# Optimization experiments

Measured on AMD Instinct MI355X. Metric: run time of the kernel, lower is better.

Reference implementation:

```python
import jax, jax.numpy as jnp
import numpy as np

EPS = 1e-7

def sphere_log(p, q):
    # Riemannian log on unit sphere; p, q broadcastable, points along last axis.
    dot = jnp.clip(jnp.sum(p * q, axis=-1, keepdims=True), -1.0 + EPS, 1.0 - EPS)
    theta = jnp.arccos(dot)
    v = q - dot * p                      # tangent direction (unnormalized)
    nv = jnp.linalg.norm(v, axis=-1, keepdims=True)
    nv_safe = jnp.where(nv < EPS, 1.0, nv)
    factor = jnp.where(nv < EPS, 1.0, theta / nv_safe)  # theta/||v|| -> 1 as q->p
    return factor * v

def sphere_exp(p, v):
    # Riemannian exp on unit sphere.
    n = jnp.linalg.norm(v, axis=-1, keepdims=True)
    n_safe = jnp.where(n < EPS, 1.0, n)
    s = jnp.where(n < EPS, 1.0, jnp.sin(n_safe) / n_safe)  # sinc(||v||)
    return jnp.cos(n) * p + s * v

def setup_inputs() -> dict:
    key = jax.random.key(0)
    k1, k2 = jax.random.split(key)
    B, L, C_in, C_out, d = 4, 256, 64, 64, 64
    x = jax.random.normal(k1, (B, L, C_in, d), dtype=jnp.float32)
    x = x / jnp.linalg.norm(x, axis=-1, keepdims=True)  # points on S^{d-1}
    # param 'w': truncated_normal(stddev=1) with shape (n_in, n_out)
    w_raw = jax.random.truncated_normal(k2, -2.0, 2.0, (C_in, C_out), dtype=jnp.float32)
    return {"x": x, "w_raw": w_raw}

def reference(x, w_raw):
    B, L, C_in, d = x.shape
    C_out = w_raw.shape[1]
    # softmax-like positive, column-normalized weights
    w = jnp.exp(w_raw - np.log(C_in).astype(np.float32))
    w = w / w.sum(axis=0)[None]          # (C_in, C_out)

    xr = x.reshape(B * L, C_in, d)       # (N, C_in, d)
    # init at first in-channel point, broadcast over out channels: (N, C_out, d)
    a = jnp.broadcast_to(xr[:, 0][:, None, :], (B * L, C_out, d))

    # 3-step fixed-point iteration toward weighted Frechet mean (scan unroll=3)
    for _ in range(3):
        logs = sphere_log(a[:, :, None, :], xr[:, None, :, :])  # (N, C_out, C_in, d)
        grad = jnp.einsum('io,noid->nod', w, logs)              # (N, C_out, d)
        a = sphere_exp(a, grad)

    return a.reshape(B, L, C_out, d)
```

## Files before the change

kernel.cpp:

```cpp
#include <hip/hip_runtime.h>

#define EPSF 1e-7f
#define TS2 72

typedef __bf16 bf16;
typedef __attribute__((ext_vector_type(8))) __bf16 bf16x8;
typedef __attribute__((ext_vector_type(4))) __bf16 bf16x4;
typedef __attribute__((ext_vector_type(4))) float f32x4;

__device__ __forceinline__ float dpp_sum16(float v) {
  int x;
  x = __builtin_amdgcn_update_dpp(0, __builtin_bit_cast(int, v), 0xB1, 0xf, 0xf, true);
  v += __builtin_bit_cast(float, x);
  x = __builtin_amdgcn_update_dpp(0, __builtin_bit_cast(int, v), 0x4E, 0xf, 0xf, true);
  v += __builtin_bit_cast(float, x);
  x = __builtin_amdgcn_update_dpp(0, __builtin_bit_cast(int, v), 0x141, 0xf, 0xf, true);
  v += __builtin_bit_cast(float, x);
  x = __builtin_amdgcn_update_dpp(0, __builtin_bit_cast(int, v), 0x140, 0xf, 0xf, true);
  v += __builtin_bit_cast(float, x);
  return v;
}

__device__ __forceinline__ float fused_factor(float dot) {
  float ax = fabsf(dot);
  float q2 = __builtin_amdgcn_rsqf(1.0f + ax);
  float r2 = __builtin_amdgcn_rsqf(1.0f - ax);
  float pa = fmaf(fmaf(fmaf(-0.0187292994f, ax, 0.0742610070f), ax,
                       -0.2121144013f), ax, 1.5707288f);
  float sel = (dot < 0.0f) ? fmaf(3.14159265358979f, r2, -pa) : pa;
  return sel * q2;
}

__global__ __launch_bounds__(256, 4) void mfd_fc_mfma(
    const float* __restrict__ x, const float* __restrict__ wraw,
    float* __restrict__ out) {
  __shared__ __align__(16) char smem[3 * 64 * TS2 * sizeof(bf16)];
  bf16* Xrow = (bf16*)smem;
  bf16* Xt   = Xrow + 64 * TS2;
  bf16* AC   = Xt + 64 * TS2;

  const int n = blockIdx.x;
  const int tid = threadIdx.x;
  const int wv = tid >> 6;
  const int lane = tid & 63;
  const int ln15 = lane & 15;
  const int quad = lane >> 4;
  const int obase = 16 * wv + 4 * quad;
  const float* xn = x + (size_t)n * 4096;

#pragma unroll
  for (int t = 0; t < 4; ++t) {
    int idx = tid + t * 256;
    int i = idx >> 4;
    int c4 = (idx & 15) << 2;
    float4 v = reinterpret_cast<const float4*>(xn)[idx];
    bf16x4 b;
    b[0] = (bf16)v.x; b[1] = (bf16)v.y; b[2] = (bf16)v.z; b[3] = (bf16)v.w;
    *reinterpret_cast<bf16x4*>(&Xrow[i * TS2 + c4]) = b;
  }

  float wf[4][4];
  {
    float cs[4] = {0.f, 0.f, 0.f, 0.f};
#pragma unroll
    for (int t = 0; t < 4; ++t) {
      float4 wr = *reinterpret_cast<const float4*>(&wraw[(16 * t + ln15) * 64 + obase]);
      wf[t][0] = __expf(wr.x); wf[t][1] = __expf(wr.y);
      wf[t][2] = __expf(wr.z); wf[t][3] = __expf(wr.w);
#pragma unroll
      for (int r = 0; r < 4; ++r) cs[r] += wf[t][r];
    }
#pragma unroll
    for (int r = 0; r < 4; ++r) {
      float inv = __builtin_amdgcn_rcpf(dpp_sum16(cs[r]));
#pragma unroll
      for (int t = 0; t < 4; ++t) wf[t][r] *= inv;
    }
  }

  float a_reg[4][4];
#pragma unroll
  for (int t = 0; t < 4; ++t) {
    float v = xn[16 * t + ln15];
#pragma unroll
    for (int r = 0; r < 4; ++r) a_reg[t][r] = v;
  }

  __syncthreads();

  bf16x8 xrf[4][2];
#pragma unroll
  for (int t = 0; t < 4; ++t)
#pragma unroll
    for (int ks = 0; ks < 2; ++ks)
      xrf[t][ks] = *reinterpret_cast<const bf16x8*>(
          &Xrow[(16 * t + ln15) * TS2 + ks * 32 + quad * 8]);

  bf16x8 x0f[2];
#pragma unroll
  for (int ks = 0; ks < 2; ++ks)
    x0f[ks] = *reinterpret_cast<const bf16x8*>(&Xrow[ks * 32 + quad * 8]);

  {
    int dd = tid & 63, ih = tid >> 6;
    bf16 tmp[16];
#pragma unroll
    for (int j = 0; j < 16; ++j) tmp[j] = Xrow[(16 * ih + j) * TS2 + dd];
    *reinterpret_cast<bf16x8*>(&Xt[dd * TS2 + 16 * ih]) =
        *reinterpret_cast<bf16x8*>(&tmp[0]);
    *reinterpret_cast<bf16x8*>(&Xt[dd * TS2 + 16 * ih + 8]) =
        *reinterpret_cast<bf16x8*>(&tmp[8]);
  }

  const bf16* acbase = &AC[(16 * wv + ln15) * TS2];

  for (int it = 0; it < 3; ++it) {
    float sd[4] = {0.f, 0.f, 0.f, 0.f};
    if (it == 0) {
#pragma unroll
      for (int t = 0; t < 4; ++t) {
        float p = 0.f;
#pragma unroll
        for (int ks = 0; ks < 2; ++ks)
#pragma unroll
          for (int j = 0; j < 8; ++j)
            p = fmaf((float)xrf[t][ks][j], (float)x0f[ks][j], p);
        p += __shfl_xor(p, 16, 64);
        p += __shfl_xor(p, 32, 64);
        float d0 = __builtin_amdgcn_fmed3f(p, -1.0f + EPSF, 1.0f - EPSF);
        float f0 = fused_factor(d0);
#pragma unroll
        for (int r = 0; r < 4; ++r) {
          bf16 cb = (bf16)(wf[t][r] * f0);
          AC[(obase + r) * TS2 + 16 * t + ln15] = cb;
          sd[r] = fmaf((float)cb, d0, sd[r]);
        }
      }
    } else {
      f32x4 acc[4] = {f32x4{0,0,0,0}, f32x4{0,0,0,0}, f32x4{0,0,0,0}, f32x4{0,0,0,0}};
#pragma unroll
      for (int ks = 0; ks < 2; ++ks) {
        bf16x8 af = *reinterpret_cast<const bf16x8*>(&acbase[ks * 32 + quad * 8]);
#pragma unroll
        for (int t = 0; t < 4; ++t)
          acc[t] = __builtin_amdgcn_mfma_f32_16x16x32_bf16(af, xrf[t][ks], acc[t], 0, 0, 0);
      }
#pragma unroll
      for (int t = 0; t < 4; ++t) {
#pragma unroll
        for (int r = 0; r < 4; ++r) {
          float raw = acc[t][r];
          float dot = __builtin_amdgcn_fmed3f(raw, -1.0f + EPSF, 1.0f - EPSF);
          bf16 cb = (bf16)(wf[t][r] * fused_factor(dot));
          AC[(obase + r) * TS2 + 16 * t + ln15] = cb;
          sd[r] = fmaf((float)cb, dot, sd[r]);
        }
      }
    }
#pragma unroll
    for (int r = 0; r < 4; ++r) sd[r] = dpp_sum16(sd[r]);

    if (it == 0) __syncthreads();

    f32x4 g[4] = {f32x4{0,0,0,0}, f32x4{0,0,0,0}, f32x4{0,0,0,0}, f32x4{0,0,0,0}};
#pragma unroll
    for (int ks = 0; ks < 2; ++ks) {
      bf16x8 af = *reinterpret_cast<const bf16x8*>(&acbase[ks * 32 + quad * 8]);
#pragma unroll
      for (int t = 0; t < 4; ++t) {
        bf16x8 bfr = *reinterpret_cast<const bf16x8*>(
            &Xt[(16 * t + ln15) * TS2 + ks * 32 + quad * 8]);
        g[t] = __builtin_amdgcn_mfma_f32_16x16x32_bf16(af, bfr, g[t], 0, 0, 0);
      }
    }

    float gn2[4] = {0.f, 0.f, 0.f, 0.f};
#pragma unroll
    for (int t = 0; t < 4; ++t)
#pragma unroll
      for (int r = 0; r < 4; ++r) {
        float v = g[t][r] - sd[r] * a_reg[t][r];
        g[t][r] = v;
        gn2[r] = fmaf(v, v, gn2[r]);
      }
#pragma unroll
    for (int r = 0; r < 4; ++r) {
      float nrm = __builtin_amdgcn_sqrtf(dpp_sum16(gn2[r]));
      float rev = nrm * 0.15915494309189535f;
      float sn_ = __builtin_amdgcn_sinf(rev);
      float cn  = __builtin_amdgcn_cosf(rev);
      float sn = (nrm < EPSF) ? 1.0f : sn_ * __builtin_amdgcn_rcpf(nrm);
#pragma unroll
      for (int t = 0; t < 4; ++t)
        a_reg[t][r] = fmaf(cn, a_reg[t][r], sn * g[t][r]);
      if (it < 2) {
#pragma unroll
        for (int t = 0; t < 4; ++t)
          AC[(obase + r) * TS2 + 16 * t + ln15] = (bf16)a_reg[t][r];
      }
    }
  }

  float* outn = out + (size_t)n * 4096;
#pragma unroll
  for (int t = 0; t < 4; ++t)
#pragma unroll
    for (int r = 0; r < 4; ++r)
      outn[(obase + r) * 64 + 16 * t + ln15] = a_reg[t][r];
}

extern "C" void kernel_launch(void* const* d_in, const int* in_sizes, int n_in,
                              void* d_out, int out_size, void* d_ws, size_t ws_size,
                              hipStream_t stream) {
  const float* x = (const float*)d_in[0];
  const float* wraw = (const float*)d_in[1];
  float* out = (float*)d_out;
  (void)d_ws; (void)ws_size;

  int N = in_sizes[0] / 4096;
  mfd_fc_mfma<<<N, 256, 0, stream>>>(x, wraw, out);
}
```

Baseline: 80.59 us.

## Transpose MFMA operand roles so each lane owns one output channel

The MFMA operands are swapped so the accumulator layout puts one output channel per lane-column and four consecutive d (or input-channel) elements per lane. Per-channel reductions become a single quad shuffle-sum instead of four 16-lane DPP reductions. Per-channel sin/cos/sqrt now runs once per lane instead of four times, and the final output and the initial point load become float4 accesses. In exchange, the weight loads are scalar and strided, LDS stores into AC are per-row contiguous, and the first iteration needs extra shuffles to redistribute the dot products and factors.

```diff
diff --git a/kernel.cpp b/kernel.cpp
--- a/kernel.cpp
+++ b/kernel.cpp
@@ -8,16 +8,9 @@
 typedef __attribute__((ext_vector_type(4))) __bf16 bf16x4;
 typedef __attribute__((ext_vector_type(4))) float f32x4;
 
-__device__ __forceinline__ float dpp_sum16(float v) {
-  int x;
-  x = __builtin_amdgcn_update_dpp(0, __builtin_bit_cast(int, v), 0xB1, 0xf, 0xf, true);
-  v += __builtin_bit_cast(float, x);
-  x = __builtin_amdgcn_update_dpp(0, __builtin_bit_cast(int, v), 0x4E, 0xf, 0xf, true);
-  v += __builtin_bit_cast(float, x);
-  x = __builtin_amdgcn_update_dpp(0, __builtin_bit_cast(int, v), 0x141, 0xf, 0xf, true);
-  v += __builtin_bit_cast(float, x);
-  x = __builtin_amdgcn_update_dpp(0, __builtin_bit_cast(int, v), 0x140, 0xf, 0xf, true);
-  v += __builtin_bit_cast(float, x);
+__device__ __forceinline__ float quad_sum(float v) {
+  v += __shfl_xor(v, 16, 64);
+  v += __shfl_xor(v, 32, 64);
   return v;
 }
 
@@ -45,7 +38,8 @@
   const int lane = tid & 63;
   const int ln15 = lane & 15;
   const int quad = lane >> 4;
-  const int obase = 16 * wv + 4 * quad;
+  const int q4 = 4 * quad;
+  const int olane = 16 * wv + ln15;
   const float* xn = x + (size_t)n * 4096;
 
 #pragma unroll
@@ -59,31 +53,29 @@
     *reinterpret_cast<bf16x4*>(&Xrow[i * TS2 + c4]) = b;
   }
 
-  float wf[4][4];
+  float wf2[4][4];
   {
-    float cs[4] = {0.f, 0.f, 0.f, 0.f};
-#pragma unroll
-    for (int t = 0; t < 4; ++t) {
-      float4 wr = *reinterpret_cast<const float4*>(&wraw[(16 * t + ln15) * 64 + obase]);
-      wf[t][0] = __expf(wr.x); wf[t][1] = __expf(wr.y);
-      wf[t][2] = __expf(wr.z); wf[t][3] = __expf(wr.w);
-#pragma unroll
-      for (int r = 0; r < 4; ++r) cs[r] += wf[t][r];
-    }
-#pragma unroll
-    for (int r = 0; r < 4; ++r) {
-      float inv = __builtin_amdgcn_rcpf(dpp_sum16(cs[r]));
-#pragma unroll
-      for (int t = 0; t < 4; ++t) wf[t][r] *= inv;
-    }
+    float cs = 0.f;
+#pragma unroll
+    for (int t = 0; t < 4; ++t)
+#pragma unroll
+      for (int r = 0; r < 4; ++r) {
+        float e = __expf(wraw[(16 * t + q4 + r) * 64 + olane]);
+        wf2[t][r] = e;
+        cs += e;
+      }
+    float inv = __builtin_amdgcn_rcpf(quad_sum(cs));
+#pragma unroll
+    for (int t = 0; t < 4; ++t)
+#pragma unroll
+      for (int r = 0; r < 4; ++r) wf2[t][r] *= inv;
   }
 
   float a_reg[4][4];
 #pragma unroll
   for (int t = 0; t < 4; ++t) {
-    float v = xn[16 * t + ln15];
-#pragma unroll
-    for (int r = 0; r < 4; ++r) a_reg[t][r] = v;
+    float4 v = *reinterpret_cast<const float4*>(&xn[16 * t + q4]);
+    a_reg[t][0] = v.x; a_reg[t][1] = v.y; a_reg[t][2] = v.z; a_reg[t][3] = v.w;
   }
 
   __syncthreads();
@@ -112,11 +104,12 @@
         *reinterpret_cast<bf16x8*>(&tmp[8]);
   }
 
-  const bf16* acbase = &AC[(16 * wv + ln15) * TS2];
+  bf16* acrow = &AC[olane * TS2];
 
   for (int it = 0; it < 3; ++it) {
-    float sd[4] = {0.f, 0.f, 0.f, 0.f};
+    float sdv = 0.f;
     if (it == 0) {
+      float d0[4], f0[4];
 #pragma unroll
       for (int t = 0; t < 4; ++t) {
         float p = 0.f;
@@ -125,25 +118,29 @@
 #pragma unroll
           for (int j = 0; j < 8; ++j)
             p = fmaf((float)xrf[t][ks][j], (float)x0f[ks][j], p);
-        p += __shfl_xor(p, 16, 64);
-        p += __shfl_xor(p, 32, 64);
-        float d0 = __builtin_amdgcn_fmed3f(p, -1.0f + EPSF, 1.0f - EPSF);
-        float f0 = fused_factor(d0);
+        p = quad_sum(p);
+        d0[t] = __builtin_amdgcn_fmed3f(p, -1.0f + EPSF, 1.0f - EPSF);
+        f0[t] = fused_factor(d0[t]);
+      }
+      const int srcb = (lane & 48) + q4;
+#pragma unroll
+      for (int t = 0; t < 4; ++t)
 #pragma unroll
         for (int r = 0; r < 4; ++r) {
-          bf16 cb = (bf16)(wf[t][r] * f0);
-          AC[(obase + r) * TS2 + 16 * t + ln15] = cb;
-          sd[r] = fmaf((float)cb, d0, sd[r]);
+          float d0n = __shfl(d0[t], srcb + r, 64);
+          float f0n = __shfl(f0[t], srcb + r, 64);
+          bf16 cb = (bf16)(wf2[t][r] * f0n);
+          acrow[16 * t + q4 + r] = cb;
+          sdv = fmaf((float)cb, d0n, sdv);
         }
-      }
     } else {
       f32x4 acc[4] = {f32x4{0,0,0,0}, f32x4{0,0,0,0}, f32x4{0,0,0,0}, f32x4{0,0,0,0}};
 #pragma unroll
       for (int ks = 0; ks < 2; ++ks) {
-        bf16x8 af = *reinterpret_cast<const bf16x8*>(&acbase[ks * 32 + quad * 8]);
+        bf16x8 bfA = *reinterpret_cast<const bf16x8*>(&acrow[ks * 32 + quad * 8]);
 #pragma unroll
         for (int t = 0; t < 4; ++t)
-          acc[t] = __builtin_amdgcn_mfma_f32_16x16x32_bf16(af, xrf[t][ks], acc[t], 0, 0, 0);
+          acc[t] = __builtin_amdgcn_mfma_f32_16x16x32_bf16(xrf[t][ks], bfA, acc[t], 0, 0, 0);
       }
 #pragma unroll
       for (int t = 0; t < 4; ++t) {
@@ -151,62 +148,65 @@
         for (int r = 0; r < 4; ++r) {
           float raw = acc[t][r];
           float dot = __builtin_amdgcn_fmed3f(raw, -1.0f + EPSF, 1.0f - EPSF);
-          bf16 cb = (bf16)(wf[t][r] * fused_factor(dot));
-          AC[(obase + r) * TS2 + 16 * t + ln15] = cb;
-          sd[r] = fmaf((float)cb, dot, sd[r]);
+          bf16 cb = (bf16)(wf2[t][r] * fused_factor(dot));
+          acrow[16 * t + q4 + r] = cb;
+          sdv = fmaf((float)cb, dot, sdv);
         }
       }
     }
-#pragma unroll
-    for (int r = 0; r < 4; ++r) sd[r] = dpp_sum16(sd[r]);
+    sdv = quad_sum(sdv);
 
     if (it == 0) __syncthreads();
 
     f32x4 g[4] = {f32x4{0,0,0,0}, f32x4{0,0,0,0}, f32x4{0,0,0,0}, f32x4{0,0,0,0}};
 #pragma unroll
     for (int ks = 0; ks < 2; ++ks) {
-      bf16x8 af = *reinterpret_cast<const bf16x8*>(&acbase[ks * 32 + quad * 8]);
+      bf16x8 cf = *reinterpret_cast<const bf16x8*>(&acrow[ks * 32 + quad * 8]);
 #pragma unroll
       for (int t = 0; t < 4; ++t) {
-        bf16x8 bfr = *reinterpret_cast<const bf16x8*>(
+        bf16x8 xtf = *reinterpret_cast<const bf16x8*>(
             &Xt[(16 * t + ln15) * TS2 + ks * 32 + quad * 8]);
-        g[t] = __builtin_amdgcn_mfma_f32_16x16x32_bf16(af, bfr, g[t], 0, 0, 0);
+        g[t] = __builtin_amdgcn_mfma_f32_16x16x32_bf16(xtf, cf, g[t], 0, 0, 0);
       }
     }
 
-    float gn2[4] = {0.f, 0.f, 0.f, 0.f};
+    float gn2 = 0.f;
 #pragma unroll
     for (int t = 0; t < 4; ++t)
 #pragma unroll
       for (int r = 0; r < 4; ++r) {
-        float v = g[t][r] - sd[r] * a_reg[t][r];
+        float v = g[t][r] - sdv * a_reg[t][r];
         g[t][r] = v;
-        gn2[r] = fmaf(v, v, gn2[r]);
-      }
-#pragma unroll
-    for (int r = 0; r < 4; ++r) {
-      float nrm = __builtin_amdgcn_sqrtf(dpp_sum16(gn2[r]));
-      float rev = nrm * 0.15915494309189535f;
-      float sn_ = __builtin_amdgcn_sinf(rev);
-      float cn  = __builtin_amdgcn_cosf(rev);
-      float sn = (nrm < EPSF) ? 1.0f : sn_ * __builtin_amdgcn_rcpf(nrm);
+        gn2 = fmaf(v, v, gn2);
+      }
+    gn2 = quad_sum(gn2);
+    float nrm = __builtin_amdgcn_sqrtf(gn2);
+    float rev = nrm * 0.15915494309189535f;
+    float sn_ = __builtin_amdgcn_sinf(rev);
+    float cn  = __builtin_amdgcn_cosf(rev);
+    float sn = (nrm < EPSF) ? 1.0f : sn_ * __builtin_amdgcn_rcpf(nrm);
+#pragma unroll
+    for (int t = 0; t < 4; ++t)
+#pragma unroll
+      for (int r = 0; r < 4; ++r)
+        a_reg[t][r] = fmaf(cn, a_reg[t][r], sn * g[t][r]);
+    if (it < 2) {
 #pragma unroll
       for (int t = 0; t < 4; ++t)
-        a_reg[t][r] = fmaf(cn, a_reg[t][r], sn * g[t][r]);
-      if (it < 2) {
-#pragma unroll
-        for (int t = 0; t < 4; ++t)
-          AC[(obase + r) * TS2 + 16 * t + ln15] = (bf16)a_reg[t][r];
-      }
+#pragma unroll
+        for (int r = 0; r < 4; ++r)
+          acrow[16 * t + q4 + r] = (bf16)a_reg[t][r];
     }
   }
 
   float* outn = out + (size_t)n * 4096;
 #pragma unroll
-  for (int t = 0; t < 4; ++t)
-#pragma unroll
-    for (int r = 0; r < 4; ++r)
-      outn[(obase + r) * 64 + 16 * t + ln15] = a_reg[t][r];
+  for (int t = 0; t < 4; ++t) {
+    float4 v4;
+    v4.x = a_reg[t][0]; v4.y = a_reg[t][1];
+    v4.z = a_reg[t][2]; v4.w = a_reg[t][3];
+    *reinterpret_cast<float4*>(&outn[olane * 64 + 16 * t + q4]) = v4;
+  }
 }
 
 extern "C" void kernel_launch(void* const* d_in, const int* in_sizes, int n_in,
```

New measurement: 79.03 us. Within noise of the previous version (-1.9%).
